# Kernel tuning notes

Measured on AMD Instinct MI355X. Metric: run time of the kernel, lower is better.

## Reference

```python
import jax, jax.numpy as jnp
import numpy as np

D_MODEL = 1024
N_HEADS = 16
WINDOW = 256
SSM_N = 256
EPS = 1e-5


def _layernorm(x, g, b):
    m = x.mean(-1, keepdims=True)
    v = ((x - m) ** 2).mean(-1, keepdims=True)
    return (x - m) / jnp.sqrt(v + EPS) * g + b


def _sliding_window_attn(Q, K, V, W):
    # Q,K,V: [B,h,T,dh]; exact sliding-window causal attention (keys q-W+1..q)
    B, h, T, dh = Q.shape
    nb = T // W
    Qb = Q.reshape(B, h, nb, W, dh)
    pad = jnp.zeros((B, h, W, dh), Q.dtype)
    Kp = jnp.concatenate([pad, K], axis=2)  # [B,h,T+W,dh]
    Kprev = Kp[:, :, :T].reshape(B, h, nb, W, dh)
    Kcur = K.reshape(B, h, nb, W, dh)
    Kwin = jnp.concatenate([Kprev, Kcur], axis=3)  # [B,h,nb,2W,dh]
    Vp = jnp.concatenate([pad, V], axis=2)
    Vprev = Vp[:, :, :T].reshape(B, h, nb, W, dh)
    Vcur = V.reshape(B, h, nb, W, dh)
    Vwin = jnp.concatenate([Vprev, Vcur], axis=3)
    scores = jnp.einsum('bhnid,bhnjd->bhnij', Qb, Kwin) / jnp.sqrt(jnp.asarray(dh, Q.dtype))
    i = jnp.arange(W)[:, None]
    j = jnp.arange(2 * W)[None, :]
    blk = jnp.arange(nb)[:, None, None]
    # key global pos = blk*W - W + j ; valid iff i < j <= i+W and key pos >= 0
    mask = (j > i) & (j <= i + W) & (blk * W - W + j >= 0)  # [nb,W,2W]
    neg = jnp.asarray(jnp.finfo(scores.dtype).min, scores.dtype)
    scores = jnp.where(mask[None, None], scores, neg)
    p = jax.nn.softmax(scores, axis=-1)
    out = jnp.einsum('bhnij,bhnjd->bhnid', p, Vwin)
    return out.reshape(B, h, T, dh)


def _forward(x, ssm_state, ln1_g, ln1_b, ln2_g, ln2_b, wq, bq, wk, bk, wv, bv,
             wo, bo, wg, bg, A, Bw, Cw, w1, b1, w2, b2):
    B, T, d = x.shape
    h = N_HEADS
    dh = d // h
    xn = _layernorm(x, ln1_g, ln1_b)
    # windowed attention path
    Q = (xn @ wq + bq).reshape(B, T, h, dh).transpose(0, 2, 1, 3)
    K = (xn @ wk + bk).reshape(B, T, h, dh).transpose(0, 2, 1, 3)
    V = (xn @ wv + bv).reshape(B, T, h, dh).transpose(0, 2, 1, 3)
    ao = _sliding_window_attn(Q, K, V, WINDOW)
    y_attn = ao.transpose(0, 2, 1, 3).reshape(B, T, d) @ wo + bo
    # SSM path: s_t = tanh(A)*s_{t-1} + B x_t ; y_t = C s_t
    alpha = jnp.tanh(A)
    u = xn @ Bw  # [B,T,N]
    def step(s, u_t):
        s = alpha * s + u_t
        return s, s
    new_state, states = jax.lax.scan(step, ssm_state, u.transpose(1, 0, 2))
    y_ssm = states.transpose(1, 0, 2) @ Cw  # [B,T,d]
    # gated fusion + residual
    g = jax.nn.sigmoid(xn @ wg + bg)
    y = g * y_attn + (1.0 - g) * y_ssm
    x = x + y
    # Pre-LN MLP
    x2 = _layernorm(x, ln2_g, ln2_b)
    x = x + jax.nn.gelu(x2 @ w1 + b1, approximate=False) @ w2 + b2
    return x, new_state


def setup_inputs() -> dict:
    key = jax.random.key(0)
    ks = jax.random.split(key, 16)
    B, T, d, N = 2, 2048, D_MODEL, SSM_N
    s = 0.02
    inp = {
        'x': jax.random.normal(ks[0], (B, T, d), jnp.float32),
        'ssm_state': jnp.zeros((B, N), jnp.float32),
        'ln1_g': jnp.ones((d,), jnp.float32),
        'ln1_b': jnp.zeros((d,), jnp.float32),
        'ln2_g': jnp.ones((d,), jnp.float32),
        'ln2_b': jnp.zeros((d,), jnp.float32),
        'wq': jax.random.normal(ks[1], (d, d), jnp.float32) * s,
        'bq': jnp.zeros((d,), jnp.float32),
        'wk': jax.random.normal(ks[2], (d, d), jnp.float32) * s,
        'bk': jnp.zeros((d,), jnp.float32),
        'wv': jax.random.normal(ks[3], (d, d), jnp.float32) * s,
        'bv': jnp.zeros((d,), jnp.float32),
        'wo': jax.random.normal(ks[4], (d, d), jnp.float32) * s,
        'bo': jnp.zeros((d,), jnp.float32),
        'wg': jax.random.normal(ks[5], (d, d), jnp.float32) * s,
        'bg': jnp.zeros((d,), jnp.float32),
        'A': jax.random.uniform(ks[6], (N,), jnp.float32, -0.1, 0.1),
        'Bw': jax.random.normal(ks[7], (d, N), jnp.float32) * s,
        'Cw': jax.random.normal(ks[8], (N, d), jnp.float32) * s,
        'w1': jax.random.normal(ks[9], (d, 4 * d), jnp.float32) * s,
        'b1': jnp.zeros((4 * d,), jnp.float32),
        'w2': jax.random.normal(ks[10], (4 * d, d), jnp.float32) * s,
        'b2': jnp.zeros((d,), jnp.float32),
    }
    return inp


def reference(x, ssm_state, ln1_g, ln1_b, ln2_g, ln2_b, wq, bq, wk, bk, wv, bv,
              wo, bo, wg, bg, A, Bw, Cw, w1, b1, w2, b2):
    return _forward(x, ssm_state, ln1_g, ln1_b, ln2_g, ln2_b, wq, bq, wk, bk,
                    wv, bv, wo, bo, wg, bg, A, Bw, Cw, w1, b1, w2, b2)
```

## Files before the change

### kernel.cpp

```cpp
#include <hip/hip_runtime.h>
#include <math.h>

#define BB 2
#define TT 2048
#define DD 1024
#define HH 16
#define DH 64
#define WW 256
#define NN 256
#define ROWS (BB*TT)
#define ROWSZ ((size_t)ROWS*DD)
#define NQU 4352

typedef unsigned short u16;
typedef __attribute__((ext_vector_type(8))) short short8;
typedef __attribute__((ext_vector_type(4))) float f32x4;

__device__ __forceinline__ float bf2f(u16 h) {
    union { unsigned int u; float f; } c; c.u = ((unsigned int)h) << 16; return c.f;
}
__device__ __forceinline__ u16 f2bf(float f) {
    union { float f; unsigned int u; } c; c.f = f;
    unsigned int r = c.u + 0x7fffu + ((c.u >> 16) & 1u);
    return (u16)(r >> 16);
}

__device__ __forceinline__ void gld16(const void* g, void* l) {
    __builtin_amdgcn_global_load_lds(
        (const __attribute__((address_space(1))) void*)g,
        (__attribute__((address_space(3))) void*)l, 16, 0, 0);
}

#define WAITB(N) asm volatile("s_waitcnt vmcnt(" #N ")\n\ts_barrier" ::: "memory")

__global__ __launch_bounds__(256) void ln_kernel(const float* __restrict__ x,
                                                 const float* __restrict__ g,
                                                 const float* __restrict__ b,
                                                 u16* __restrict__ out) {
    int row = blockIdx.x;
    int t = threadIdx.x;
    const float4* xr = (const float4*)(x + (size_t)row * DD);
    float4 v4 = xr[t];
    float s  = v4.x + v4.y + v4.z + v4.w;
    float s2 = v4.x*v4.x + v4.y*v4.y + v4.z*v4.z + v4.w*v4.w;
    #pragma unroll
    for (int o = 32; o > 0; o >>= 1) { s += __shfl_xor(s, o); s2 += __shfl_xor(s2, o); }
    __shared__ float red[2][4];
    int wid = t >> 6, lane = t & 63;
    if (lane == 0) { red[0][wid] = s; red[1][wid] = s2; }
    __syncthreads();
    s  = red[0][0] + red[0][1] + red[0][2] + red[0][3];
    s2 = red[1][0] + red[1][1] + red[1][2] + red[1][3];
    float mean = s * (1.0f / DD);
    float var  = s2 * (1.0f / DD) - mean * mean;
    float inv  = rsqrtf(var + 1e-5f);
    const float4* g4 = (const float4*)g;
    const float4* b4 = (const float4*)b;
    float4 gg = g4[t], bb = b4[t];
    float o0 = (v4.x - mean) * inv * gg.x + bb.x;
    float o1 = (v4.y - mean) * inv * gg.y + bb.y;
    float o2 = (v4.z - mean) * inv * gg.z + bb.z;
    float o3 = (v4.w - mean) * inv * gg.w + bb.w;
    uint2 packed;
    packed.x = (unsigned)f2bf(o0) | ((unsigned)f2bf(o1) << 16);
    packed.y = (unsigned)f2bf(o2) | ((unsigned)f2bf(o3) << 16);
    *(uint2*)(out + (size_t)row * DD + 4 * t) = packed;
}

__global__ __launch_bounds__(256) void tconv_all(
    const float* __restrict__ wq, const float* __restrict__ wk,
    const float* __restrict__ wv, const float* __restrict__ wg,
    const float* __restrict__ Bw, const float* __restrict__ wo,
    const float* __restrict__ Cw, const float* __restrict__ w1,
    const float* __restrict__ w2,
    u16* __restrict__ wqkvgut, u16* __restrict__ wot, u16* __restrict__ cwt,
    u16* __restrict__ w1t, u16* __restrict__ w2t) {
    int tile = blockIdx.x;
    const float* src; u16* dst; int K, N, tx, ty;
    if (tile < 4096) {
        int seg = tile >> 10, tl = tile & 1023;
        src = (seg == 0) ? wq : (seg == 1) ? wk : (seg == 2) ? wv : wg;
        dst = wqkvgut + (size_t)seg * 1024 * 1024;
        K = 1024; N = 1024; tx = tl & 31; ty = tl >> 5;
    } else if (tile < 4352) {
        int tl = tile - 4096;
        src = Bw; dst = wqkvgut + (size_t)4096 * 1024;
        K = 1024; N = 256; tx = tl & 7; ty = tl >> 3;
    } else if (tile < 5376) {
        int tl = tile - 4352;
        src = wo; dst = wot; K = 1024; N = 1024; tx = tl & 31; ty = tl >> 5;
    } else if (tile < 5632) {
        int tl = tile - 5376;
        src = Cw; dst = cwt; K = 256; N = 1024; tx = tl & 31; ty = tl >> 5;
    } else if (tile < 9728) {
        int tl = tile - 5632;
        src = w1; dst = w1t; K = 1024; N = 4096; tx = tl & 127; ty = tl >> 7;
    } else {
        int tl = tile - 9728;
        src = w2; dst = w2t; K = 4096; N = 1024; tx = tl & 31; ty = tl >> 5;
    }
    __shared__ float ts[32][33];
    int n0 = tx * 32, k0 = ty * 32;
    int tc = threadIdx.x & 31, tr = threadIdx.x >> 5;
    #pragma unroll
    for (int i = tr; i < 32; i += 8)
        ts[i][tc] = src[(size_t)(k0 + i) * N + n0 + tc];
    __syncthreads();
    #pragma unroll
    for (int i = tr; i < 32; i += 8)
        dst[(size_t)(n0 + i) * K + k0 + tc] = f2bf(ts[tc][i]);
}

__global__ __launch_bounds__(256) void bias_init(const float* __restrict__ bq,
                                                 const float* __restrict__ bk,
                                                 const float* __restrict__ bv,
                                                 const float* __restrict__ bg,
                                                 float* __restrict__ dst) {
    int i = blockIdx.x * 256 + threadIdx.x;
    if (i >= NQU) return;
    float v = 0.f;
    if (i < 1024) v = bq[i];
    else if (i < 2048) v = bk[i - 1024];
    else if (i < 3072) v = bv[i - 2048];
    else if (i < 4096) v = bg[i - 3072];
    dst[i] = v;
}

__device__ __forceinline__ void gemm_core_pipe(const u16* __restrict__ A,
                                               const u16* __restrict__ Bt,
                                               int K, int kiters, int kofs,
                                               int m0, int n0,
                                               short (*Als)[128][32],
                                               short (*Bls)[128][32],
                                               int t, f32x4 acc[4][4]) {
    int lane = t & 63, w = t >> 6;
    int wr = w >> 1, wc = w & 1;
    int jq = lane >> 4, rq = lane & 15;
    int swzb = (jq ^ ((rq >> 1) & 3)) << 4;
    const char* gA[2]; const char* gB[2];
    int lofs[2];
    #pragma unroll
    for (int i = 0; i < 2; i++) {
        int s = i * 256 + t;
        int r = s >> 2, p = s & 3;
        int j = p ^ ((r >> 1) & 3);
        gA[i] = (const char*)(A + (size_t)(m0 + r) * K + kofs) + j * 16;
        gB[i] = (const char*)(Bt + (size_t)(n0 + r) * K + kofs) + j * 16;
        lofs[i] = s * 16;
    }
    #pragma unroll
    for (int i = 0; i < 2; i++) {
        gld16(gA[i], (char*)(Als + 0) + lofs[i]);
        gld16(gB[i], (char*)(Bls + 0) + lofs[i]);
    }
    if (kiters > 1) {
        #pragma unroll
        for (int i = 0; i < 2; i++) {
            gld16(gA[i] + 64, (char*)(Als + 1) + lofs[i]);
            gld16(gB[i] + 64, (char*)(Bls + 1) + lofs[i]);
        }
    }
    for (int kt = 0; kt < kiters; kt++) {
        if (kt + 1 < kiters) { WAITB(4); } else { WAITB(0); }
        if (kt + 2 < kiters) {
            int q = (kt + 2) % 3;
            size_t ko = (size_t)(kt + 2) * 64;
            #pragma unroll
            for (int i = 0; i < 2; i++) {
                gld16(gA[i] + ko, (char*)(Als + q) + lofs[i]);
                gld16(gB[i] + ko, (char*)(Bls + q) + lofs[i]);
            }
        }
        int p = kt % 3;
        const char* Ab = (const char*)(Als + p);
        const char* Bb = (const char*)(Bls + p);
        short8 af[4], bfr[4];
        #pragma unroll
        for (int i = 0; i < 4; i++) {
            af[i]  = *(const short8*)(Ab + (wr * 64 + i * 16 + rq) * 64 + swzb);
            bfr[i] = *(const short8*)(Bb + (wc * 64 + i * 16 + rq) * 64 + swzb);
        }
        #pragma unroll
        for (int i = 0; i < 4; i++)
            #pragma unroll
            for (int jn = 0; jn < 4; jn++)
                acc[i][jn] = __builtin_amdgcn_mfma_f32_16x16x32_bf16(af[i], bfr[jn], acc[i][jn], 0, 0, 0);
    }
}

template<int ACT, bool OUTBF, bool SPLIT>
__global__ __launch_bounds__(256) void mgemm64(const u16* __restrict__ A,
                                               const u16* __restrict__ Bt,
                                               const float* __restrict__ bias,
                                               void* __restrict__ C,
                                               int M, int N, int K, int Kslice,
                                               int mtiles, int ntiles, int PM, int PN) {
    __shared__ __align__(16) short Als[3][128][32];
    __shared__ __align__(16) short Bls[3][128][32];
    int t = threadIdx.x;
    int l = blockIdx.x;
    int xcd = l & 7, li = l >> 3;
    int rm = mtiles / PM, rn = ntiles / PN;
    int xm = xcd % PM, xn = xcd / PM;
    int mt = xm * rm + li % rm;
    int nt = xn * rn + li / rm;
    int m0 = mt * 128, n0 = nt * 128;
    int z = SPLIT ? blockIdx.y : 0;
    f32x4 acc[4][4];
    #pragma unroll
    for (int i = 0; i < 4; i++)
        #pragma unroll
        for (int j = 0; j < 4; j++)
            acc[i][j] = (f32x4){0.f, 0.f, 0.f, 0.f};
    gemm_core_pipe(A, Bt, K, Kslice >> 5, z * Kslice, m0, n0, Als, Bls, t, acc);

    int lane = t & 63, w = t >> 6;
    int wr = w >> 1, wc = w & 1;
    int jq = lane >> 4, rq = lane & 15;
    u16* Cb = OUTBF ? ((u16*)C + (SPLIT ? (size_t)z * M * N : (size_t)0)) : nullptr;
    float* Cf = (float*)C;
    #pragma unroll
    for (int i = 0; i < 4; i++) {
        int rowb = m0 + wr * 64 + i * 16 + jq * 4;
        #pragma unroll
        for (int jn = 0; jn < 4; jn++) {
            int col = n0 + wc * 64 + jn * 16 + rq;
            float bv = bias ? bias[col] : 0.f;
            #pragma unroll
            for (int rr = 0; rr < 4; rr++) {
                float v = acc[i][jn][rr] + bv;
                if (ACT == 1) v = 0.5f * v * (1.0f + erff(v * 0.70710678118654752f));
                size_t off = (size_t)(rowb + rr) * N + col;
                if (OUTBF) Cb[off] = f2bf(v);
                else Cf[off] = v;
            }
        }
    }
}

__global__ __launch_bounds__(256) void proj3(const u16* __restrict__ ao,
                                             const u16* __restrict__ states,
                                             const u16* __restrict__ wot,
                                             const u16* __restrict__ cwt,
                                             const float* __restrict__ bo,
                                             u16* __restrict__ ya0,
                                             u16* __restrict__ ya1,
                                             float* __restrict__ ys) {
    __shared__ __align__(16) short Als[3][128][32];
    __shared__ __align__(16) short Bls[3][128][32];
    int t = threadIdx.x;
    int m0 = blockIdx.y * 128, n0 = blockIdx.x * 128;
    int z = blockIdx.z;
    const u16* A; const u16* Bt; int K, kofs, kiters;
    if (z < 2) { A = ao; Bt = wot; K = 1024; kofs = z * 512; kiters = 16; }
    else       { A = states; Bt = cwt; K = 256; kofs = 0; kiters = 8; }
    f32x4 acc[4][4];
    #pragma unroll
    for (int i = 0; i < 4; i++)
        #pragma unroll
        for (int j = 0; j < 4; j++)
            acc[i][j] = (f32x4){0.f, 0.f, 0.f, 0.f};
    gemm_core_pipe(A, Bt, K, kiters, kofs, m0, n0, Als, Bls, t, acc);

    int lane = t & 63, w = t >> 6;
    int wr = w >> 1, wc = w & 1;
    int jq = lane >> 4, rq = lane & 15;
    u16* dst = (z == 0) ? ya0 : ya1;
    #pragma unroll
    for (int i = 0; i < 4; i++) {
        int rowb = m0 + wr * 64 + i * 16 + jq * 4;
        #pragma unroll
        for (int jn = 0; jn < 4; jn++) {
            int col = n0 + wc * 64 + jn * 16 + rq;
            float bv = (z == 0) ? bo[col] : 0.f;
            #pragma unroll
            for (int rr = 0; rr < 4; rr++) {
                float v = acc[i][jn][rr] + bv;
                size_t off = (size_t)(rowb + rr) * DD + col;
                if (z < 2) dst[off] = f2bf(v);
                else ys[off] = v;
            }
        }
    }
}

__global__ __launch_bounds__(256) void attn_scan(const u16* __restrict__ QKVG,
                                                 u16* __restrict__ O,
                                                 const float* __restrict__ Assm,
                                                 const float* __restrict__ s0,
                                                 u16* __restrict__ states,
                                                 float* __restrict__ s_out) {
    __shared__ __align__(16) short Qs[8][64][8];
    __shared__ __align__(16) short Ks[8][64][8];
    __shared__ __align__(16) short Vt[64][72];
    __shared__ __align__(16) short Ps[4][16][72];

    if (blockIdx.x >= 1024) {
        int idx = (blockIdx.x - 1024) * 256 + threadIdx.x;
        int n = idx & 255;
        int c = (idx >> 8) & 31;
        int b = idx >> 13;
        float alpha = tanhf(Assm[n]);
        int t0 = c * 64;
        float s = (c == 0) ? s0[b * NN + n] : 0.f;
        const u16* up = QKVG + (size_t)(b * TT) * NQU + 4096 + n;
        if (c > 0) {
            #pragma unroll
            for (int k = 8; k >= 1; k--)
                s = alpha * s + bf2f(up[(size_t)(t0 - k) * NQU]);
        }
        u16* sp = states + (size_t)(b * TT) * NN + n;
        for (int t = t0; t < t0 + 64; t++) {
            s = alpha * s + bf2f(up[(size_t)t * NQU]);
            sp[(size_t)t * NN] = f2bf(s);
        }
        if (c == 31) s_out[b * NN + n] = s;
        return;
    }

    int blk = blockIdx.x;
    int qb = blk & 31;
    int h  = (blk >> 5) & 15;
    int b  = blk >> 9;
    int q0 = qb * 64;
    int t = threadIdx.x, lane = t & 63, w = t >> 6;
    int rq = lane & 15, jq = lane >> 4;

    const size_t RS = NQU;

    #pragma unroll
    for (int i = 0; i < 2; i++) {
        int c = 2 * w + i;
        const u16* g = QKVG + (size_t)(b * TT + q0 + lane) * RS + h * 64 + c * 8;
        gld16(g, (char*)Qs + c * 1024);
    }

    f32x4 Oa[4];
    #pragma unroll
    for (int tj = 0; tj < 4; tj++) Oa[tj] = (f32x4){0.f, 0.f, 0.f, 0.f};
    float mrow[4], lrow[4];
    #pragma unroll
    for (int r = 0; r < 4; r++) { mrow[r] = -1e30f; lrow[r] = 0.f; }

    int c0 = 4 - (q0 >> 6); if (c0 < 0) c0 = 0;

    for (int ci = c0; ci < 5; ci++) {
        int kbase = q0 - 256 + ci * 64;
        #pragma unroll
        for (int i = 0; i < 2; i++) {
            int c = 2 * w + i;
            const u16* g = QKVG + (size_t)(b * TT + kbase + lane) * RS + 1024 + h * 64 + c * 8;
            gld16(g, (char*)Ks + c * 1024);
        }
        #pragma unroll
        for (int i = 0; i < 2; i++) {
            int dhg = i * 4 + w;
            uint4 v = *(const uint4*)(QKVG + (size_t)(b * TT + kbase + lane) * RS + 2048 + h * 64 + dhg * 8);
            const u16* pv = (const u16*)&v;
            #pragma unroll
            for (int j = 0; j < 8; j++) Vt[dhg * 8 + j][lane] = (short)pv[j];
        }
        __syncthreads();

        short8 qf[2];
        #pragma unroll
        for (int s = 0; s < 2; s++)
            qf[s] = *(const short8*)&Qs[4 * s + jq][w * 16 + rq][0];

        f32x4 S[4];
        #pragma unroll
        for (int tj = 0; tj < 4; tj++) S[tj] = (f32x4){0.f, 0.f, 0.f, 0.f};
        #pragma unroll
        for (int s = 0; s < 2; s++)
            #pragma unroll
            for (int tj = 0; tj < 4; tj++) {
                short8 kf = *(const short8*)&Ks[4 * s + jq][tj * 16 + rq][0];
                S[tj] = __builtin_amdgcn_mfma_f32_16x16x32_bf16(qf[s], kf, S[tj], 0, 0, 0);
            }

        #pragma unroll
        for (int r = 0; r < 4; r++) {
            int q = q0 + w * 16 + jq * 4 + r;
            float sv[4];
            #pragma unroll
            for (int tj = 0; tj < 4; tj++) {
                int kp = kbase + tj * 16 + rq;
                float x = S[tj][r] * 0.125f;
                bool valid = (kp <= q) && (kp > q - WW);
                sv[tj] = valid ? x : -1e30f;
            }
            float cm = fmaxf(fmaxf(sv[0], sv[1]), fmaxf(sv[2], sv[3]));
            #pragma unroll
            for (int o = 1; o < 16; o <<= 1) cm = fmaxf(cm, __shfl_xor(cm, o));
            float mn = fmaxf(mrow[r], cm);
            bool any = mn > -1e29f;
            float al = any ? __expf(mrow[r] - mn) : 1.f;
            float ps = 0.f;
            #pragma unroll
            for (int tj = 0; tj < 4; tj++) {
                float p = any ? __expf(sv[tj] - mn) : 0.f;
                ps += p;
                Ps[w][jq * 4 + r][tj * 16 + rq] = (short)f2bf(p);
            }
            #pragma unroll
            for (int o = 1; o < 16; o <<= 1) ps += __shfl_xor(ps, o);
            lrow[r] = lrow[r] * al + ps;
            mrow[r] = mn;
            #pragma unroll
            for (int tj = 0; tj < 4; tj++) Oa[tj][r] *= al;
        }

        #pragma unroll
        for (int s = 0; s < 2; s++) {
            short8 pf = *(const short8*)&Ps[w][rq][32 * s + 8 * jq];
            #pragma unroll
            for (int tj = 0; tj < 4; tj++) {
                short8 vf = *(const short8*)&Vt[tj * 16 + rq][32 * s + 8 * jq];
                Oa[tj] = __builtin_amdgcn_mfma_f32_16x16x32_bf16(pf, vf, Oa[tj], 0, 0, 0);
            }
        }
        __syncthreads();
    }

    #pragma unroll
    for (int r = 0; r < 4; r++) {
        int q = q0 + w * 16 + jq * 4 + r;
        float inv = 1.f / lrow[r];
        #pragma unroll
        for (int tj = 0; tj < 4; tj++)
            O[(size_t)(b * TT + q) * DD + h * 64 + tj * 16 + rq] = f2bf(Oa[tj][r] * inv);
    }
}

__global__ __launch_bounds__(256) void fuse_ln2(const float* __restrict__ x,
                                                const u16* __restrict__ QKVG,
                                                const u16* __restrict__ ya0,
                                                const u16* __restrict__ ya1,
                                                const float* __restrict__ ys,
                                                const float* __restrict__ g2,
                                                const float* __restrict__ b2,
                                                float* __restrict__ out,
                                                u16* __restrict__ x2n) {
    int row = blockIdx.x, t = threadIdx.x;
    float4 xv = ((const float4*)(x + (size_t)row * DD))[t];
    uint2 gw = *(const uint2*)(QKVG + (size_t)row * NQU + 3072 + 4 * t);
    uint2 a0 = *(const uint2*)(ya0 + (size_t)row * DD + 4 * t);
    uint2 a1 = *(const uint2*)(ya1 + (size_t)row * DD + 4 * t);
    float4 sv = ((const float4*)(ys + (size_t)row * DD))[t];
    u16 gh[4] = {(u16)(gw.x & 0xffff), (u16)(gw.x >> 16), (u16)(gw.y & 0xffff), (u16)(gw.y >> 16)};
    u16 ah[4] = {(u16)(a0.x & 0xffff), (u16)(a0.x >> 16), (u16)(a0.y & 0xffff), (u16)(a0.y >> 16)};
    u16 bh[4] = {(u16)(a1.x & 0xffff), (u16)(a1.x >> 16), (u16)(a1.y & 0xffff), (u16)(a1.y >> 16)};
    float xe[4] = {xv.x, xv.y, xv.z, xv.w};
    float se[4] = {sv.x, sv.y, sv.z, sv.w};
    float o[4];
    #pragma unroll
    for (int e = 0; e < 4; e++) {
        float g = 1.0f / (1.0f + __expf(-bf2f(gh[e])));
        float a = bf2f(ah[e]) + bf2f(bh[e]);
        o[e] = xe[e] + g * a + (1.0f - g) * se[e];
    }
    float s = o[0] + o[1] + o[2] + o[3];
    float s2 = o[0]*o[0] + o[1]*o[1] + o[2]*o[2] + o[3]*o[3];
    #pragma unroll
    for (int off = 32; off > 0; off >>= 1) { s += __shfl_xor(s, off); s2 += __shfl_xor(s2, off); }
    __shared__ float red[2][4];
    int wid = t >> 6, lane = t & 63;
    if (lane == 0) { red[0][wid] = s; red[1][wid] = s2; }
    __syncthreads();
    s  = red[0][0] + red[0][1] + red[0][2] + red[0][3];
    s2 = red[1][0] + red[1][1] + red[1][2] + red[1][3];
    float mean = s * (1.0f / DD);
    float var  = s2 * (1.0f / DD) - mean * mean;
    float inv  = rsqrtf(var + 1e-5f);
    float4 gg = ((const float4*)g2)[t];
    float4 bb = ((const float4*)b2)[t];
    float ge[4] = {gg.x, gg.y, gg.z, gg.w};
    float be[4] = {bb.x, bb.y, bb.z, bb.w};
    float4 ov = {o[0], o[1], o[2], o[3]};
    ((float4*)(out + (size_t)row * DD))[t] = ov;
    u16 nh[4];
    #pragma unroll
    for (int e = 0; e < 4; e++) nh[e] = f2bf((o[e] - mean) * inv * ge[e] + be[e]);
    uint2 packed;
    packed.x = (unsigned)nh[0] | ((unsigned)nh[1] << 16);
    packed.y = (unsigned)nh[2] | ((unsigned)nh[3] << 16);
    *(uint2*)(x2n + (size_t)row * DD + 4 * t) = packed;
}

__global__ __launch_bounds__(256) void mlp2_reduce(const u16* __restrict__ pbase,
                                                   const float* __restrict__ b2,
                                                   float* __restrict__ out) {
    size_t i4 = (size_t)blockIdx.x * 256 + threadIdx.x;
    float4 o = ((float4*)out)[i4];
    float4 bb = ((const float4*)b2)[i4 & 255];
    float acc0 = bb.x, acc1 = bb.y, acc2 = bb.z, acc3 = bb.w;
    #pragma unroll
    for (int z = 0; z < 4; z++) {
        uint2 p = ((const uint2*)(pbase + (size_t)z * ROWSZ))[i4];
        acc0 += bf2f((u16)(p.x & 0xffff));
        acc1 += bf2f((u16)(p.x >> 16));
        acc2 += bf2f((u16)(p.y & 0xffff));
        acc3 += bf2f((u16)(p.y >> 16));
    }
    o.x += acc0; o.y += acc1; o.z += acc2; o.w += acc3;
    ((float4*)out)[i4] = o;
}

extern "C" void kernel_launch(void* const* d_in, const int* in_sizes, int n_in,
                              void* d_out, int out_size, void* d_ws, size_t ws_size,
                              hipStream_t stream) {
    const float* x     = (const float*)d_in[0];
    const float* sst   = (const float*)d_in[1];
    const float* ln1g  = (const float*)d_in[2];
    const float* ln1b  = (const float*)d_in[3];
    const float* ln2g  = (const float*)d_in[4];
    const float* ln2b  = (const float*)d_in[5];
    const float* wq    = (const float*)d_in[6];
    const float* bq    = (const float*)d_in[7];
    const float* wk    = (const float*)d_in[8];
    const float* bk    = (const float*)d_in[9];
    const float* wv    = (const float*)d_in[10];
    const float* bv    = (const float*)d_in[11];
    const float* wo    = (const float*)d_in[12];
    const float* bo    = (const float*)d_in[13];
    const float* wg    = (const float*)d_in[14];
    const float* bg    = (const float*)d_in[15];
    const float* A     = (const float*)d_in[16];
    const float* Bw    = (const float*)d_in[17];
    const float* Cw    = (const float*)d_in[18];
    const float* w1    = (const float*)d_in[19];
    const float* b1    = (const float*)d_in[20];
    const float* w2    = (const float*)d_in[21];
    const float* b2    = (const float*)d_in[22];

    float* out = (float*)d_out;
    char* ws = (char*)d_ws;
    const size_t KBs = 1024;

    u16*   QKVGU  = (u16*)(ws);
    u16*   ya0b   = (u16*)(ws + 34816 * KBs);
    u16*   ya1b   = (u16*)(ws + 43008 * KBs);
    float* ys     = (float*)(ws + 51200 * KBs);
    u16*   parts  = ya0b;
    u16*   xn     = (u16*)(ws + 67584 * KBs);
    u16*   ao     = (u16*)(ws + 75776 * KBs);
    u16*   states = (u16*)(ws + 83968 * KBs);
    u16*   wqkvgut= (u16*)(ws + 86016 * KBs);
    u16*   wot    = (u16*)(ws + 94720 * KBs);
    u16*   cwt    = (u16*)(ws + 96768 * KBs);
    u16*   w1t    = (u16*)(ws + 97280 * KBs);
    u16*   w2t    = (u16*)(ws + 105472 * KBs);
    float* biasq  = (float*)(ws + 113664 * KBs);
    u16*   x2n    = xn;
    u16*   h1     = QKVGU;

    float* new_state_out = out + ROWSZ;

    hipLaunchKernelGGL(tconv_all, dim3(13824), dim3(256), 0, stream,
                       wq, wk, wv, wg, Bw, wo, Cw, w1, w2,
                       wqkvgut, wot, cwt, w1t, w2t);
    hipLaunchKernelGGL(bias_init, dim3(17), dim3(256), 0, stream, bq, bk, bv, bg, biasq);

    hipLaunchKernelGGL(ln_kernel, dim3(ROWS), dim3(256), 0, stream, x, ln1g, ln1b, xn);
    hipLaunchKernelGGL((mgemm64<0,true,false>), dim3(1088, 1), dim3(256), 0, stream,
                       xn, wqkvgut, biasq, (void*)QKVGU, ROWS, NQU, 1024, 1024,
                       32, 34, 4, 2);
    hipLaunchKernelGGL(attn_scan, dim3(1088), dim3(256), 0, stream,
                       QKVGU, ao, A, sst, states, new_state_out);
    hipLaunchKernelGGL(proj3, dim3(8, 32, 3), dim3(256), 0, stream,
                       ao, states, wot, cwt, bo, ya0b, ya1b, ys);
    hipLaunchKernelGGL(fuse_ln2, dim3(ROWS), dim3(256), 0, stream,
                       x, QKVGU, ya0b, ya1b, ys, ln2g, ln2b, out, x2n);
    hipLaunchKernelGGL((mgemm64<1,true,false>), dim3(1024, 1), dim3(256), 0, stream,
                       x2n, w1t, b1, (void*)h1, ROWS, 4*DD, 1024, 1024,
                       32, 32, 4, 2);
    hipLaunchKernelGGL((mgemm64<0,true,true>), dim3(256, 4), dim3(256), 0, stream,
                       h1, w2t, (const float*)nullptr, (void*)parts, ROWS, DD, 4096, 1024,
                       32, 8, 8, 1);
    hipLaunchKernelGGL(mlp2_reduce, dim3(4096), dim3(256), 0, stream, parts, b2, out);
}
```

Measured before the change: 422.7 us.

## Replace triple-buffered K=32 GEMM pipeline with double-buffered K=64 tiles

The shared GEMM core now loads 64-wide K tiles into two LDS buffers instead of 32-wide tiles into three. Each iteration prefetches the next tile, runs two MFMA k-substeps from the current one, and ends with a __syncthreads. The LDS swizzle is widened to 8 chunks to match, and iteration counts are halved. The aim is fewer barriers and more MFMA work per sync. In exchange it drops the explicit vmcnt-based wait that let loads stay in flight across more than one stage, which may expose more global-load latency.

```diff
diff --git a/kernel.cpp b/kernel.cpp
--- a/kernel.cpp
+++ b/kernel.cpp
@@ -30,8 +30,6 @@
         (const __attribute__((address_space(1))) void*)g,
         (__attribute__((address_space(3))) void*)l, 16, 0, 0);
 }
-
-#define WAITB(N) asm volatile("s_waitcnt vmcnt(" #N ")\n\ts_barrier" ::: "memory")
 
 __global__ __launch_bounds__(256) void ln_kernel(const float* __restrict__ x,
                                                  const float* __restrict__ g,
@@ -126,65 +124,73 @@
     dst[i] = v;
 }
 
-__device__ __forceinline__ void gemm_core_pipe(const u16* __restrict__ A,
-                                               const u16* __restrict__ Bt,
-                                               int K, int kiters, int kofs,
-                                               int m0, int n0,
-                                               short (*Als)[128][32],
-                                               short (*Bls)[128][32],
-                                               int t, f32x4 acc[4][4]) {
+__device__ __forceinline__ void gemm_core_2ph(const u16* __restrict__ A,
+                                              const u16* __restrict__ Bt,
+                                              int K, int kiters, int kofs,
+                                              int m0, int n0,
+                                              short (*Als)[128][64],
+                                              short (*Bls)[128][64],
+                                              int t, f32x4 acc[4][4]) {
     int lane = t & 63, w = t >> 6;
     int wr = w >> 1, wc = w & 1;
     int jq = lane >> 4, rq = lane & 15;
-    int swzb = (jq ^ ((rq >> 1) & 3)) << 4;
-    const char* gA[2]; const char* gB[2];
-    int lofs[2];
-    #pragma unroll
-    for (int i = 0; i < 2; i++) {
+    const char* gA[4]; const char* gB[4]; int lofs[4];
+    #pragma unroll
+    for (int i = 0; i < 4; i++) {
         int s = i * 256 + t;
-        int r = s >> 2, p = s & 3;
-        int j = p ^ ((r >> 1) & 3);
+        int r = s >> 3, p = s & 7;
+        int j = p ^ (r & 7);
         gA[i] = (const char*)(A + (size_t)(m0 + r) * K + kofs) + j * 16;
         gB[i] = (const char*)(Bt + (size_t)(n0 + r) * K + kofs) + j * 16;
         lofs[i] = s * 16;
     }
-    #pragma unroll
-    for (int i = 0; i < 2; i++) {
+    int rowA[4], rowB[4];
+    #pragma unroll
+    for (int i = 0; i < 4; i++) {
+        rowA[i] = (wr * 64 + i * 16 + rq) * 128;
+        rowB[i] = (wc * 64 + i * 16 + rq) * 128;
+    }
+    int csw[2];
+    #pragma unroll
+    for (int ks = 0; ks < 2; ks++)
+        csw[ks] = ((ks * 4 + jq) ^ (rq & 7)) << 4;
+
+    #pragma unroll
+    for (int i = 0; i < 4; i++) {
         gld16(gA[i], (char*)(Als + 0) + lofs[i]);
         gld16(gB[i], (char*)(Bls + 0) + lofs[i]);
     }
-    if (kiters > 1) {
-        #pragma unroll
-        for (int i = 0; i < 2; i++) {
-            gld16(gA[i] + 64, (char*)(Als + 1) + lofs[i]);
-            gld16(gB[i] + 64, (char*)(Bls + 1) + lofs[i]);
-        }
-    }
+    __syncthreads();
+
     for (int kt = 0; kt < kiters; kt++) {
-        if (kt + 1 < kiters) { WAITB(4); } else { WAITB(0); }
-        if (kt + 2 < kiters) {
-            int q = (kt + 2) % 3;
-            size_t ko = (size_t)(kt + 2) * 64;
-            #pragma unroll
-            for (int i = 0; i < 2; i++) {
-                gld16(gA[i] + ko, (char*)(Als + q) + lofs[i]);
-                gld16(gB[i] + ko, (char*)(Bls + q) + lofs[i]);
-            }
-        }
-        int p = kt % 3;
-        const char* Ab = (const char*)(Als + p);
-        const char* Bb = (const char*)(Bls + p);
-        short8 af[4], bfr[4];
-        #pragma unroll
-        for (int i = 0; i < 4; i++) {
-            af[i]  = *(const short8*)(Ab + (wr * 64 + i * 16 + rq) * 64 + swzb);
-            bfr[i] = *(const short8*)(Bb + (wc * 64 + i * 16 + rq) * 64 + swzb);
-        }
-        #pragma unroll
-        for (int i = 0; i < 4; i++)
-            #pragma unroll
-            for (int jn = 0; jn < 4; jn++)
-                acc[i][jn] = __builtin_amdgcn_mfma_f32_16x16x32_bf16(af[i], bfr[jn], acc[i][jn], 0, 0, 0);
+        int cur = kt & 1;
+        if (kt + 1 < kiters) {
+            size_t ko = (size_t)(kt + 1) * 128;
+            int nxt = cur ^ 1;
+            #pragma unroll
+            for (int i = 0; i < 4; i++) {
+                gld16(gA[i] + ko, (char*)(Als + nxt) + lofs[i]);
+                gld16(gB[i] + ko, (char*)(Bls + nxt) + lofs[i]);
+            }
+        }
+        const char* Ab = (const char*)(Als + cur);
+        const char* Bb = (const char*)(Bls + cur);
+        short8 af[2][4], bfr[2][4];
+        #pragma unroll
+        for (int ks = 0; ks < 2; ks++)
+            #pragma unroll
+            for (int i = 0; i < 4; i++) {
+                af[ks][i]  = *(const short8*)(Ab + rowA[i] + csw[ks]);
+                bfr[ks][i] = *(const short8*)(Bb + rowB[i] + csw[ks]);
+            }
+        #pragma unroll
+        for (int ks = 0; ks < 2; ks++)
+            #pragma unroll
+            for (int i = 0; i < 4; i++)
+                #pragma unroll
+                for (int jn = 0; jn < 4; jn++)
+                    acc[i][jn] = __builtin_amdgcn_mfma_f32_16x16x32_bf16(af[ks][i], bfr[ks][jn], acc[i][jn], 0, 0, 0);
+        __syncthreads();
     }
 }
 
@@ -195,8 +201,8 @@
                                                void* __restrict__ C,
                                                int M, int N, int K, int Kslice,
                                                int mtiles, int ntiles, int PM, int PN) {
-    __shared__ __align__(16) short Als[3][128][32];
-    __shared__ __align__(16) short Bls[3][128][32];
+    __shared__ __align__(16) short Als[2][128][64];
+    __shared__ __align__(16) short Bls[2][128][64];
     int t = threadIdx.x;
     int l = blockIdx.x;
     int xcd = l & 7, li = l >> 3;
@@ -212,7 +218,7 @@
         #pragma unroll
         for (int j = 0; j < 4; j++)
             acc[i][j] = (f32x4){0.f, 0.f, 0.f, 0.f};
-    gemm_core_pipe(A, Bt, K, Kslice >> 5, z * Kslice, m0, n0, Als, Bls, t, acc);
+    gemm_core_2ph(A, Bt, K, Kslice >> 6, z * Kslice, m0, n0, Als, Bls, t, acc);
 
     int lane = t & 63, w = t >> 6;
     int wr = w >> 1, wc = w & 1;
@@ -246,21 +252,21 @@
                                              u16* __restrict__ ya0,
                                              u16* __restrict__ ya1,
                                              float* __restrict__ ys) {
-    __shared__ __align__(16) short Als[3][128][32];
-    __shared__ __align__(16) short Bls[3][128][32];
+    __shared__ __align__(16) short Als[2][128][64];
+    __shared__ __align__(16) short Bls[2][128][64];
     int t = threadIdx.x;
     int m0 = blockIdx.y * 128, n0 = blockIdx.x * 128;
     int z = blockIdx.z;
     const u16* A; const u16* Bt; int K, kofs, kiters;
-    if (z < 2) { A = ao; Bt = wot; K = 1024; kofs = z * 512; kiters = 16; }
-    else       { A = states; Bt = cwt; K = 256; kofs = 0; kiters = 8; }
+    if (z < 2) { A = ao; Bt = wot; K = 1024; kofs = z * 512; kiters = 8; }
+    else       { A = states; Bt = cwt; K = 256; kofs = 0; kiters = 4; }
     f32x4 acc[4][4];
     #pragma unroll
     for (int i = 0; i < 4; i++)
         #pragma unroll
         for (int j = 0; j < 4; j++)
             acc[i][j] = (f32x4){0.f, 0.f, 0.f, 0.f};
-    gemm_core_pipe(A, Bt, K, kiters, kofs, m0, n0, Als, Bls, t, acc);
+    gemm_core_2ph(A, Bt, K, kiters, kofs, m0, n0, Als, Bls, t, acc);
 
     int lane = t & 63, w = t >> 6;
     int wr = w >> 1, wc = w & 1;
```

New measurement: 388.9 us. 8.0% less time.

## Switch GEMMs to 256x256 tiles with 8-wave 4-stage pipeline and split SSM input projection

Applied to the files above, without the earlier changes.

The GEMM core moves from 128x128 tiles on 4 waves with a 3-stage buffer to 256x256 tiles on 8 waves with a 4-stage LDS ring. Loads for B and A are interleaved between two half-MFMA phases, with barriers and s_setprio, so more data is reused per load and memory latency hides behind compute. The SSM input projection (N=256) no longer rides on the QKVG GEMM. It gets its own split-K GEMM plus a reduce kernel, so the main GEMM N becomes 4096 and divides evenly into 256 tiles. The trade-offs are fewer blocks, higher register and LDS use per block, and an extra launch plus a bf16 partial-sum round trip.

```diff
diff --git a/kernel.cpp b/kernel.cpp
--- a/kernel.cpp
+++ b/kernel.cpp
@@ -10,7 +10,6 @@
 #define NN 256
 #define ROWS (BB*TT)
 #define ROWSZ ((size_t)ROWS*DD)
-#define NQU 4352
 
 typedef unsigned short u16;
 typedef __attribute__((ext_vector_type(8))) short short8;
@@ -30,8 +29,6 @@
         (const __attribute__((address_space(1))) void*)g,
         (__attribute__((address_space(3))) void*)l, 16, 0, 0);
 }
-
-#define WAITB(N) asm volatile("s_waitcnt vmcnt(" #N ")\n\ts_barrier" ::: "memory")
 
 __global__ __launch_bounds__(256) void ln_kernel(const float* __restrict__ x,
                                                  const float* __restrict__ g,
@@ -117,86 +114,98 @@
                                                  const float* __restrict__ bg,
                                                  float* __restrict__ dst) {
     int i = blockIdx.x * 256 + threadIdx.x;
-    if (i >= NQU) return;
-    float v = 0.f;
+    if (i >= 4096) return;
+    float v;
     if (i < 1024) v = bq[i];
     else if (i < 2048) v = bk[i - 1024];
     else if (i < 3072) v = bv[i - 2048];
-    else if (i < 4096) v = bg[i - 3072];
+    else v = bg[i - 3072];
     dst[i] = v;
 }
 
-__device__ __forceinline__ void gemm_core_pipe(const u16* __restrict__ A,
-                                               const u16* __restrict__ Bt,
-                                               int K, int kiters, int kofs,
-                                               int m0, int n0,
-                                               short (*Als)[128][32],
-                                               short (*Bls)[128][32],
-                                               int t, f32x4 acc[4][4]) {
-    int lane = t & 63, w = t >> 6;
-    int wr = w >> 1, wc = w & 1;
+#define ATILE 16384
+
+__device__ __forceinline__ void gemm_core_d3(const u16* __restrict__ A,
+                                             const u16* __restrict__ Bt,
+                                             int K, int kiters, int kofs,
+                                             int m0, int n0,
+                                             char* Als, char* Bls,
+                                             int t, f32x4 acc[8][4]) {
+    int lane = t & 63, wid = t >> 6;
+    int wm = wid >> 2, wn = wid & 3;
     int jq = lane >> 4, rq = lane & 15;
-    int swzb = (jq ^ ((rq >> 1) & 3)) << 4;
-    const char* gA[2]; const char* gB[2];
-    int lofs[2];
-    #pragma unroll
-    for (int i = 0; i < 2; i++) {
-        int s = i * 256 + t;
+    int csw = (jq ^ (rq & 3)) << 4;
+    int rowA[8], rowB[4];
+    #pragma unroll
+    for (int i = 0; i < 8; i++) rowA[i] = (i * 32 + wm * 16 + rq) * 64;
+    #pragma unroll
+    for (int j = 0; j < 4; j++) rowB[j] = (wn * 64 + j * 16 + rq) * 64;
+
+    const char* gA[2]; const char* gB[2]; int lof[2];
+    #pragma unroll
+    for (int c = 0; c < 2; c++) {
+        int s = c * 512 + t;
         int r = s >> 2, p = s & 3;
-        int j = p ^ ((r >> 1) & 3);
-        gA[i] = (const char*)(A + (size_t)(m0 + r) * K + kofs) + j * 16;
-        gB[i] = (const char*)(Bt + (size_t)(n0 + r) * K + kofs) + j * 16;
-        lofs[i] = s * 16;
-    }
-    #pragma unroll
-    for (int i = 0; i < 2; i++) {
-        gld16(gA[i], (char*)(Als + 0) + lofs[i]);
-        gld16(gB[i], (char*)(Bls + 0) + lofs[i]);
-    }
-    if (kiters > 1) {
-        #pragma unroll
-        for (int i = 0; i < 2; i++) {
-            gld16(gA[i] + 64, (char*)(Als + 1) + lofs[i]);
-            gld16(gB[i] + 64, (char*)(Bls + 1) + lofs[i]);
-        }
-    }
+        int j = p ^ (r & 3);
+        gA[c] = (const char*)(A + (size_t)(m0 + r) * K + kofs) + j * 16;
+        gB[c] = (const char*)(Bt + (size_t)(n0 + r) * K + kofs) + j * 16;
+        lof[c] = s * 16;
+    }
+
+#define STB(q) { size_t ko=(size_t)(q)*64; char* d=Bls+((q)&3)*ATILE; gld16(gB[0]+ko,d+lof[0]); gld16(gB[1]+ko,d+lof[1]); }
+#define STA(q) { size_t ko=(size_t)(q)*64; char* d=Als+((q)&3)*ATILE; gld16(gA[0]+ko,d+lof[0]); gld16(gA[1]+ko,d+lof[1]); }
+
+    STB(0) STA(0) STB(1) STA(1) STB(2) STA(2)
+    asm volatile("s_waitcnt vmcnt(8)\n\ts_barrier" ::: "memory");
+
     for (int kt = 0; kt < kiters; kt++) {
-        if (kt + 1 < kiters) { WAITB(4); } else { WAITB(0); }
-        if (kt + 2 < kiters) {
-            int q = (kt + 2) % 3;
-            size_t ko = (size_t)(kt + 2) * 64;
-            #pragma unroll
-            for (int i = 0; i < 2; i++) {
-                gld16(gA[i] + ko, (char*)(Als + q) + lofs[i]);
-                gld16(gB[i] + ko, (char*)(Bls + q) + lofs[i]);
-            }
-        }
-        int p = kt % 3;
-        const char* Ab = (const char*)(Als + p);
-        const char* Bb = (const char*)(Bls + p);
-        short8 af[4], bfr[4];
-        #pragma unroll
-        for (int i = 0; i < 4; i++) {
-            af[i]  = *(const short8*)(Ab + (wr * 64 + i * 16 + rq) * 64 + swzb);
-            bfr[i] = *(const short8*)(Bb + (wc * 64 + i * 16 + rq) * 64 + swzb);
-        }
+        const char* Ab = Als + (kt & 3) * ATILE;
+        const char* Bb = Bls + (kt & 3) * ATILE;
+        bool st = (kt + 3 < kiters);
+        short8 bfr[4], af[4];
+        #pragma unroll
+        for (int j = 0; j < 4; j++) bfr[j] = *(const short8*)(Bb + rowB[j] + csw);
+        #pragma unroll
+        for (int i = 0; i < 4; i++) af[i] = *(const short8*)(Ab + rowA[i] + csw);
+        if (st) STB(kt + 3)
+        asm volatile("s_barrier" ::: "memory");
+        __builtin_amdgcn_s_setprio(1);
         #pragma unroll
         for (int i = 0; i < 4; i++)
             #pragma unroll
-            for (int jn = 0; jn < 4; jn++)
-                acc[i][jn] = __builtin_amdgcn_mfma_f32_16x16x32_bf16(af[i], bfr[jn], acc[i][jn], 0, 0, 0);
-    }
+            for (int j = 0; j < 4; j++)
+                acc[i][j] = __builtin_amdgcn_mfma_f32_16x16x32_bf16(af[i], bfr[j], acc[i][j], 0, 0, 0);
+        __builtin_amdgcn_s_setprio(0);
+        asm volatile("s_barrier" ::: "memory");
+        #pragma unroll
+        for (int i = 0; i < 4; i++) af[i] = *(const short8*)(Ab + rowA[4 + i] + csw);
+        if (st) STA(kt + 3)
+        asm volatile("s_barrier" ::: "memory");
+        __builtin_amdgcn_s_setprio(1);
+        #pragma unroll
+        for (int i = 0; i < 4; i++)
+            #pragma unroll
+            for (int j = 0; j < 4; j++)
+                acc[4 + i][j] = __builtin_amdgcn_mfma_f32_16x16x32_bf16(af[i], bfr[j], acc[4 + i][j], 0, 0, 0);
+        __builtin_amdgcn_s_setprio(0);
+        if (st)                   { asm volatile("s_waitcnt vmcnt(8)\n\ts_barrier" ::: "memory"); }
+        else if (kt + 2 < kiters) { asm volatile("s_waitcnt vmcnt(4)\n\ts_barrier" ::: "memory"); }
+        else if (kt + 1 < kiters) { asm volatile("s_waitcnt vmcnt(0)\n\ts_barrier" ::: "memory"); }
+        else                      { asm volatile("s_barrier" ::: "memory"); }
+    }
+#undef STB
+#undef STA
 }
 
 template<int ACT, bool OUTBF, bool SPLIT>
-__global__ __launch_bounds__(256) void mgemm64(const u16* __restrict__ A,
-                                               const u16* __restrict__ Bt,
-                                               const float* __restrict__ bias,
-                                               void* __restrict__ C,
-                                               int M, int N, int K, int Kslice,
-                                               int mtiles, int ntiles, int PM, int PN) {
-    __shared__ __align__(16) short Als[3][128][32];
-    __shared__ __align__(16) short Bls[3][128][32];
+__global__ __launch_bounds__(512, 2) void mgemm64(const u16* __restrict__ A,
+                                                  const u16* __restrict__ Bt,
+                                                  const float* __restrict__ bias,
+                                                  void* __restrict__ C,
+                                                  int M, int N, int K, int Kslice,
+                                                  int mtiles, int ntiles, int PM, int PN) {
+    __shared__ __align__(16) char Als[4 * ATILE];
+    __shared__ __align__(16) char Bls[4 * ATILE];
     int t = threadIdx.x;
     int l = blockIdx.x;
     int xcd = l & 7, li = l >> 3;
@@ -204,27 +213,27 @@
     int xm = xcd % PM, xn = xcd / PM;
     int mt = xm * rm + li % rm;
     int nt = xn * rn + li / rm;
-    int m0 = mt * 128, n0 = nt * 128;
+    int m0 = mt * 256, n0 = nt * 256;
     int z = SPLIT ? blockIdx.y : 0;
-    f32x4 acc[4][4];
-    #pragma unroll
-    for (int i = 0; i < 4; i++)
+    f32x4 acc[8][4];
+    #pragma unroll
+    for (int i = 0; i < 8; i++)
         #pragma unroll
         for (int j = 0; j < 4; j++)
             acc[i][j] = (f32x4){0.f, 0.f, 0.f, 0.f};
-    gemm_core_pipe(A, Bt, K, Kslice >> 5, z * Kslice, m0, n0, Als, Bls, t, acc);
-
-    int lane = t & 63, w = t >> 6;
-    int wr = w >> 1, wc = w & 1;
+    gemm_core_d3(A, Bt, K, Kslice >> 5, z * Kslice, m0, n0, Als, Bls, t, acc);
+
+    int lane = t & 63, wid = t >> 6;
+    int wm = wid >> 2, wn = wid & 3;
     int jq = lane >> 4, rq = lane & 15;
     u16* Cb = OUTBF ? ((u16*)C + (SPLIT ? (size_t)z * M * N : (size_t)0)) : nullptr;
     float* Cf = (float*)C;
     #pragma unroll
-    for (int i = 0; i < 4; i++) {
-        int rowb = m0 + wr * 64 + i * 16 + jq * 4;
+    for (int i = 0; i < 8; i++) {
+        int rowb = m0 + i * 32 + wm * 16 + jq * 4;
         #pragma unroll
         for (int jn = 0; jn < 4; jn++) {
-            int col = n0 + wc * 64 + jn * 16 + rq;
+            int col = n0 + wn * 64 + jn * 16 + rq;
             float bv = bias ? bias[col] : 0.f;
             #pragma unroll
             for (int rr = 0; rr < 4; rr++) {
@@ -238,40 +247,58 @@
     }
 }
 
-__global__ __launch_bounds__(256) void proj3(const u16* __restrict__ ao,
-                                             const u16* __restrict__ states,
-                                             const u16* __restrict__ wot,
-                                             const u16* __restrict__ cwt,
-                                             const float* __restrict__ bo,
-                                             u16* __restrict__ ya0,
-                                             u16* __restrict__ ya1,
-                                             float* __restrict__ ys) {
-    __shared__ __align__(16) short Als[3][128][32];
-    __shared__ __align__(16) short Bls[3][128][32];
+__global__ __launch_bounds__(256) void ureduce(const u16* __restrict__ p,
+                                               u16* __restrict__ o) {
+    size_t i2 = (size_t)blockIdx.x * 256 + threadIdx.x;
+    float a0 = 0.f, a1 = 0.f, a2 = 0.f, a3 = 0.f;
+    #pragma unroll
+    for (int z = 0; z < 8; z++) {
+        uint2 v = ((const uint2*)(p + (size_t)z * 1048576))[i2];
+        a0 += bf2f((u16)(v.x & 0xffff));
+        a1 += bf2f((u16)(v.x >> 16));
+        a2 += bf2f((u16)(v.y & 0xffff));
+        a3 += bf2f((u16)(v.y >> 16));
+    }
+    uint2 r;
+    r.x = (unsigned)f2bf(a0) | ((unsigned)f2bf(a1) << 16);
+    r.y = (unsigned)f2bf(a2) | ((unsigned)f2bf(a3) << 16);
+    ((uint2*)o)[i2] = r;
+}
+
+__global__ __launch_bounds__(512, 2) void proj3(const u16* __restrict__ ao,
+                                                const u16* __restrict__ states,
+                                                const u16* __restrict__ wot,
+                                                const u16* __restrict__ cwt,
+                                                const float* __restrict__ bo,
+                                                u16* __restrict__ ya0,
+                                                u16* __restrict__ ya1,
+                                                float* __restrict__ ys) {
+    __shared__ __align__(16) char Als[4 * ATILE];
+    __shared__ __align__(16) char Bls[4 * ATILE];
     int t = threadIdx.x;
-    int m0 = blockIdx.y * 128, n0 = blockIdx.x * 128;
+    int m0 = blockIdx.y * 256, n0 = blockIdx.x * 256;
     int z = blockIdx.z;
     const u16* A; const u16* Bt; int K, kofs, kiters;
     if (z < 2) { A = ao; Bt = wot; K = 1024; kofs = z * 512; kiters = 16; }
     else       { A = states; Bt = cwt; K = 256; kofs = 0; kiters = 8; }
-    f32x4 acc[4][4];
-    #pragma unroll
-    for (int i = 0; i < 4; i++)
+    f32x4 acc[8][4];
+    #pragma unroll
+    for (int i = 0; i < 8; i++)
         #pragma unroll
         for (int j = 0; j < 4; j++)
             acc[i][j] = (f32x4){0.f, 0.f, 0.f, 0.f};
-    gemm_core_pipe(A, Bt, K, kiters, kofs, m0, n0, Als, Bls, t, acc);
-
-    int lane = t & 63, w = t >> 6;
-    int wr = w >> 1, wc = w & 1;
+    gemm_core_d3(A, Bt, K, kiters, kofs, m0, n0, Als, Bls, t, acc);
+
+    int lane = t & 63, wid = t >> 6;
+    int wm = wid >> 2, wn = wid & 3;
     int jq = lane >> 4, rq = lane & 15;
     u16* dst = (z == 0) ? ya0 : ya1;
     #pragma unroll
-    for (int i = 0; i < 4; i++) {
-        int rowb = m0 + wr * 64 + i * 16 + jq * 4;
+    for (int i = 0; i < 8; i++) {
+        int rowb = m0 + i * 32 + wm * 16 + jq * 4;
         #pragma unroll
         for (int jn = 0; jn < 4; jn++) {
-            int col = n0 + wc * 64 + jn * 16 + rq;
+            int col = n0 + wn * 64 + jn * 16 + rq;
             float bv = (z == 0) ? bo[col] : 0.f;
             #pragma unroll
             for (int rr = 0; rr < 4; rr++) {
@@ -285,6 +312,7 @@
 }
 
 __global__ __launch_bounds__(256) void attn_scan(const u16* __restrict__ QKVG,
+                                                 const u16* __restrict__ ubuf,
                                                  u16* __restrict__ O,
                                                  const float* __restrict__ Assm,
                                                  const float* __restrict__ s0,
@@ -303,15 +331,15 @@
         float alpha = tanhf(Assm[n]);
         int t0 = c * 64;
         float s = (c == 0) ? s0[b * NN + n] : 0.f;
-        const u16* up = QKVG + (size_t)(b * TT) * NQU + 4096 + n;
+        const u16* up = ubuf + (size_t)(b * TT) * NN + n;
         if (c > 0) {
             #pragma unroll
             for (int k = 8; k >= 1; k--)
-                s = alpha * s + bf2f(up[(size_t)(t0 - k) * NQU]);
+                s = alpha * s + bf2f(up[(size_t)(t0 - k) * NN]);
         }
         u16* sp = states + (size_t)(b * TT) * NN + n;
         for (int t = t0; t < t0 + 64; t++) {
-            s = alpha * s + bf2f(up[(size_t)t * NQU]);
+            s = alpha * s + bf2f(up[(size_t)t * NN]);
             sp[(size_t)t * NN] = f2bf(s);
         }
         if (c == 31) s_out[b * NN + n] = s;
@@ -326,7 +354,7 @@
     int t = threadIdx.x, lane = t & 63, w = t >> 6;
     int rq = lane & 15, jq = lane >> 4;
 
-    const size_t RS = NQU;
+    const size_t RS = 4096;
 
     #pragma unroll
     for (int i = 0; i < 2; i++) {
@@ -443,7 +471,7 @@
                                                 u16* __restrict__ x2n) {
     int row = blockIdx.x, t = threadIdx.x;
     float4 xv = ((const float4*)(x + (size_t)row * DD))[t];
-    uint2 gw = *(const uint2*)(QKVG + (size_t)row * NQU + 3072 + 4 * t);
+    uint2 gw = *(const uint2*)(QKVG + (size_t)row * 4096 + 3072 + 4 * t);
     uint2 a0 = *(const uint2*)(ya0 + (size_t)row * DD + 4 * t);
     uint2 a1 = *(const uint2*)(ya1 + (size_t)row * DD + 4 * t);
     float4 sv = ((const float4*)(ys + (size_t)row * DD))[t];
@@ -537,10 +565,11 @@
     char* ws = (char*)d_ws;
     const size_t KBs = 1024;
 
-    u16*   QKVGU  = (u16*)(ws);
+    u16*   QKVG   = (u16*)(ws);
     u16*   ya0b   = (u16*)(ws + 34816 * KBs);
     u16*   ya1b   = (u16*)(ws + 43008 * KBs);
     float* ys     = (float*)(ws + 51200 * KBs);
+    u16*   uparts = ya0b;
     u16*   parts  = ya0b;
     u16*   xn     = (u16*)(ws + 67584 * KBs);
     u16*   ao     = (u16*)(ws + 75776 * KBs);
@@ -552,30 +581,36 @@
     u16*   w2t    = (u16*)(ws + 105472 * KBs);
     float* biasq  = (float*)(ws + 113664 * KBs);
     u16*   x2n    = xn;
-    u16*   h1     = QKVGU;
+    u16*   ubuf   = xn;
+    u16*   h1     = QKVG;
 
     float* new_state_out = out + ROWSZ;
 
     hipLaunchKernelGGL(tconv_all, dim3(13824), dim3(256), 0, stream,
                        wq, wk, wv, wg, Bw, wo, Cw, w1, w2,
                        wqkvgut, wot, cwt, w1t, w2t);
-    hipLaunchKernelGGL(bias_init, dim3(17), dim3(256), 0, stream, bq, bk, bv, bg, biasq);
+    hipLaunchKernelGGL(bias_init, dim3(16), dim3(256), 0, stream, bq, bk, bv, bg, biasq);
 
     hipLaunchKernelGGL(ln_kernel, dim3(ROWS), dim3(256), 0, stream, x, ln1g, ln1b, xn);
-    hipLaunchKernelGGL((mgemm64<0,true,false>), dim3(1088, 1), dim3(256), 0, stream,
-                       xn, wqkvgut, biasq, (void*)QKVGU, ROWS, NQU, 1024, 1024,
-                       32, 34, 4, 2);
+    hipLaunchKernelGGL((mgemm64<0,true,false>), dim3(256, 1), dim3(512), 0, stream,
+                       xn, wqkvgut, biasq, (void*)QKVG, ROWS, 4096, 1024, 1024,
+                       16, 16, 4, 2);
+    hipLaunchKernelGGL((mgemm64<0,true,true>), dim3(16, 8), dim3(512), 0, stream,
+                       xn, wqkvgut + (size_t)4096 * 1024, (const float*)nullptr,
+                       (void*)uparts, ROWS, 256, 1024, 128,
+                       16, 1, 8, 1);
+    hipLaunchKernelGGL(ureduce, dim3(1024), dim3(256), 0, stream, uparts, ubuf);
     hipLaunchKernelGGL(attn_scan, dim3(1088), dim3(256), 0, stream,
-                       QKVGU, ao, A, sst, states, new_state_out);
-    hipLaunchKernelGGL(proj3, dim3(8, 32, 3), dim3(256), 0, stream,
+                       QKVG, ubuf, ao, A, sst, states, new_state_out);
+    hipLaunchKernelGGL(proj3, dim3(4, 16, 3), dim3(512), 0, stream,
                        ao, states, wot, cwt, bo, ya0b, ya1b, ys);
     hipLaunchKernelGGL(fuse_ln2, dim3(ROWS), dim3(256), 0, stream,
-                       x, QKVGU, ya0b, ya1b, ys, ln2g, ln2b, out, x2n);
-    hipLaunchKernelGGL((mgemm64<1,true,false>), dim3(1024, 1), dim3(256), 0, stream,
+                       x, QKVG, ya0b, ya1b, ys, ln2g, ln2b, out, x2n);
+    hipLaunchKernelGGL((mgemm64<1,true,false>), dim3(256, 1), dim3(512), 0, stream,
                        x2n, w1t, b1, (void*)h1, ROWS, 4*DD, 1024, 1024,
-                       32, 32, 4, 2);
-    hipLaunchKernelGGL((mgemm64<0,true,true>), dim3(256, 4), dim3(256), 0, stream,
+                       16, 16, 4, 2);
+    hipLaunchKernelGGL((mgemm64<0,true,true>), dim3(64, 4), dim3(512), 0, stream,
                        h1, w2t, (const float*)nullptr, (void*)parts, ROWS, DD, 4096, 1024,
-                       32, 8, 8, 1);
+                       16, 4, 8, 1);
     hipLaunchKernelGGL(mlp2_reduce, dim3(4096), dim3(256), 0, stream, parts, b2, out);
 }
```

New measurement: 411.4 us. -2.7%, faster.
